# Kernel optimization log

Hardware: AMD Instinct MI355X
Metric: run time of the kernel (lower is better)

The kernel has to match this reference:

```python
import jax, jax.numpy as jnp
import numpy as np

P = 16           # patch size
D = 768          # embed / feature dim (= 3*P*P)
T = 8            # number of task vectors
H_META = 192     # MetaNet hidden (= D // 4)


def patchify(x):
    # x: [B, 3, H, W] -> [B, N, 3*P*P]
    B, C, H, W = x.shape
    x = x.reshape(B, C, H // P, P, W // P, P)
    x = x.transpose(0, 2, 4, 1, 3, 5)
    return x.reshape(B, (H // P) * (W // P), C * P * P)


def encode(W1, b1, W2, b2, x):
    # base functional encoder f(params, x): shared weights over the batch
    patches = patchify(x)                       # [B, N, D]
    h = jax.nn.relu(patches @ W1 + b1)          # [B, N, D]
    pooled = h.mean(axis=1)                     # [B, D]
    return pooled @ W2 + b2                     # [B, D]


def setup_inputs() -> dict:
    key = jax.random.key(0)
    ks = jax.random.split(key, 14)
    B = 64
    s = 0.02
    return {
        "x":   jax.random.normal(ks[0], (B, 3, 224, 224), jnp.float32),
        # base model params
        "W1":  jax.random.normal(ks[1], (D, D), jnp.float32) * s,
        "b1":  jax.random.normal(ks[2], (D,), jnp.float32) * s,
        "W2":  jax.random.normal(ks[3], (D, D), jnp.float32) * s,
        "b2":  jax.random.normal(ks[4], (D,), jnp.float32) * s,
        # task-vector deltas (stacked over T tasks)
        "dW1": jax.random.normal(ks[5], (T, D, D), jnp.float32) * s,
        "db1": jax.random.normal(ks[6], (T, D), jnp.float32) * s,
        "dW2": jax.random.normal(ks[7], (T, D, D), jnp.float32) * s,
        "db2": jax.random.normal(ks[8], (T, D), jnp.float32) * s,
        # MetaNet (Linear-ReLU-Linear); zero-init in the original, random here
        "mw1": jax.random.normal(ks[9], (D, H_META), jnp.float32) * s,
        "mb1": jax.random.normal(ks[10], (H_META,), jnp.float32) * s,
        "mw2": jax.random.normal(ks[11], (H_META, T), jnp.float32) * s,
        "mb2": jax.random.normal(ks[12], (T,), jnp.float32) * s,
    }


def reference(x, W1, b1, W2, b2, dW1, db1, dW2, db2, mw1, mb1, mw2, mb2):
    # 1) base features with frozen base model (torch.no_grad)
    base = jax.lax.stop_gradient(encode(W1, b1, W2, b2, x))       # [B, D]
    # 2) per-sample mixing coefficients via MetaNet
    coefs = jax.nn.relu(base @ mw1 + mb1) @ mw2 + mb2             # [B, T]
    # 3) per-sample mixed parameters: p + sum_t c[b,t] * dp[t]
    nW1 = W1 + jnp.einsum("bt,tij->bij", coefs, dW1)              # [B, D, D]
    nb1 = b1 + coefs @ db1                                        # [B, D]
    nW2 = W2 + jnp.einsum("bt,tij->bij", coefs, dW2)              # [B, D, D]
    nb2 = b2 + coefs @ db2                                        # [B, D]
    # 4) batched per-sample forward with the mixed weights
    patches = patchify(x)                                         # [B, N, D]
    h = jax.nn.relu(jnp.einsum("bnd,bde->bne", patches, nW1) + nb1[:, None, :])
    pooled = h.mean(axis=1)                                       # [B, D]
    out = jnp.einsum("bd,bde->be", pooled, nW2) + nb2             # [B, D]
    return out
```

## Files before the change

kernel.cpp:

```cpp
#include <hip/hip_runtime.h>
#include <hip/hip_bf16.h>


typedef __bf16 bf16x8 __attribute__((ext_vector_type(8)));
typedef float f32x4 __attribute__((ext_vector_type(4)));

struct alignas(16) BF8 { __hip_bfloat16 h[8]; };

constexpr int BATCH = 64;
constexpr int NP    = 196;
constexpr int NPAD  = 256;
constexpr int DIM   = 768;
constexpr int NT    = 8;
constexpr int HM    = 192;
constexpr size_t MSZ = (size_t)DIM * DIM;

__global__ void k_patchify(const float* __restrict__ x, __hip_bfloat16* __restrict__ A) {
  int idx  = blockIdx.x * blockDim.x + threadIdx.x;
  int col4 = idx % (DIM / 4);
  int row  = idx / (DIM / 4);
  int d = col4 * 4;
  int b = row >> 8;
  int n = row & 255;
  __hip_bfloat16 tmp[4];
  if (n < NP) {
    int hp = n / 14, wp = n % 14;
    int c  = d >> 8;
    int rr = d & 255;
    int i = rr >> 4, j = rr & 15;
    const float* src = x + ((((size_t)b * 3 + c) * 224 + hp * 16 + i) * 224 + wp * 16 + j);
    float4 f = *(const float4*)src;
    tmp[0] = __float2bfloat16(f.x);
    tmp[1] = __float2bfloat16(f.y);
    tmp[2] = __float2bfloat16(f.z);
    tmp[3] = __float2bfloat16(f.w);
  } else {
    tmp[0] = tmp[1] = tmp[2] = tmp[3] = __float2bfloat16(0.0f);
  }
  *(ushort4*)(A + (size_t)row * DIM + d) = *(ushort4*)tmp;
}

__global__ void k_transpose_cast(const float* __restrict__ W1, const float* __restrict__ dW1,
                                 const float* __restrict__ W2, const float* __restrict__ dW2,
                                 __hip_bfloat16* __restrict__ WT) {
  __shared__ float tile[32][33];
  int mat = blockIdx.z;
  const float* src;
  if      (mat == 0) src = W1;
  else if (mat <= 8) src = dW1 + (size_t)(mat - 1) * MSZ;
  else if (mat == 9) src = W2;
  else               src = dW2 + (size_t)(mat - 10) * MSZ;
  int n0 = blockIdx.x * 32;
  int k0 = blockIdx.y * 32;
  int tx = threadIdx.x & 31, ty = threadIdx.x >> 5;
#pragma unroll
  for (int r = ty; r < 32; r += 8)
    tile[r][tx] = src[(size_t)(k0 + r) * DIM + n0 + tx];
  __syncthreads();
  __hip_bfloat16* dst = WT + (size_t)mat * MSZ;
#pragma unroll
  for (int r = ty; r < 32; r += 8)
    dst[(size_t)(n0 + r) * DIM + k0 + tx] = __float2bfloat16(tile[tx][r]);
}

constexpr int LDP = 40;

__global__ __launch_bounds__(256, 2)
void k_gemm_pool(const __hip_bfloat16* __restrict__ A,
                 const __hip_bfloat16* __restrict__ WT,
                 const float* __restrict__ b1,
                 const float* __restrict__ db1,
                 const float* __restrict__ coefs,
                 __hip_bfloat16* __restrict__ pooled) {
  __shared__ __hip_bfloat16 Asl[256][LDP];
  __shared__ __hip_bfloat16 Bsl[64][LDP];
  __shared__ float biasl[64];
  __shared__ float cl[NT];
  __shared__ float red[4][64];

  int b  = blockIdx.x;
  int n0 = blockIdx.y * 64;
  int tid = threadIdx.x;

  if (tid < NT) cl[tid] = coefs ? coefs[b * NT + tid] : 0.0f;
  __syncthreads();
  if (tid < 64) {
    float bias = b1[n0 + tid];
    if (coefs) {
#pragma unroll
      for (int t = 0; t < NT; t++) bias += cl[t] * db1[t * DIM + n0 + tid];
    }
    biasl[tid] = bias;
  }

  int wave = tid >> 6, lane = tid & 63;
  int quad = lane >> 4, l16 = lane & 15;
  f32x4 acc[4][4] = {};
  const __hip_bfloat16* Ag = A + (size_t)b * (NPAD * DIM);

  for (int k0 = 0; k0 < DIM; k0 += 32) {
    {
      int kl = (tid & 3) * 8;
      int r  = tid >> 2;
#pragma unroll
      for (int p = 0; p < 4; p++, r += 64)
        *(uint4*)(&Asl[r][kl]) = *(const uint4*)(Ag + (size_t)r * DIM + k0 + kl);
    }
    {
      int kl = (tid & 3) * 8;
      int nl = tid >> 2;
      const __hip_bfloat16* p0 = WT + (size_t)(n0 + nl) * DIM + k0 + kl;
      if (coefs) {
        BF8 w = *(const BF8*)p0;
        float m[8];
#pragma unroll
        for (int i = 0; i < 8; i++) m[i] = __bfloat162float(w.h[i]);
#pragma unroll
        for (int t = 0; t < NT; t++) {
          BF8 dv = *(const BF8*)(p0 + (size_t)(1 + t) * MSZ);
          float c = cl[t];
#pragma unroll
          for (int i = 0; i < 8; i++) m[i] += c * __bfloat162float(dv.h[i]);
        }
        BF8 o;
#pragma unroll
        for (int i = 0; i < 8; i++) o.h[i] = __float2bfloat16(m[i]);
        *(BF8*)(&Bsl[nl][kl]) = o;
      } else {
        *(uint4*)(&Bsl[nl][kl]) = *(const uint4*)p0;
      }
    }
    __syncthreads();
    int m0 = wave * 64;
    bf16x8 af[4], bfr[4];
#pragma unroll
    for (int mf = 0; mf < 4; mf++)
      af[mf] = *(const bf16x8*)(&Asl[m0 + mf * 16 + l16][quad * 8]);
#pragma unroll
    for (int nf = 0; nf < 4; nf++)
      bfr[nf] = *(const bf16x8*)(&Bsl[nf * 16 + l16][quad * 8]);
#pragma unroll
    for (int mf = 0; mf < 4; mf++)
#pragma unroll
      for (int nf = 0; nf < 4; nf++)
        acc[mf][nf] = __builtin_amdgcn_mfma_f32_16x16x32_bf16(af[mf], bfr[nf], acc[mf][nf], 0, 0, 0);
    __syncthreads();
  }

  int m0 = wave * 64;
  float colsum[4];
#pragma unroll
  for (int nf = 0; nf < 4; nf++) {
    float bias = biasl[nf * 16 + l16];
    float s = 0.0f;
#pragma unroll
    for (int mf = 0; mf < 4; mf++) {
      int rowbase = m0 + mf * 16 + quad * 4;
#pragma unroll
      for (int r = 0; r < 4; r++) {
        if (rowbase + r < NP) s += fmaxf(acc[mf][nf][r] + bias, 0.0f);
      }
    }
    s += __shfl_xor(s, 16, 64);
    s += __shfl_xor(s, 32, 64);
    colsum[nf] = s;
  }
  if (lane < 16) {
#pragma unroll
    for (int nf = 0; nf < 4; nf++) red[wave][nf * 16 + lane] = colsum[nf];
  }
  __syncthreads();
  if (tid < 64) {
    float s = red[0][tid] + red[1][tid] + red[2][tid] + red[3][tid];
    pooled[(size_t)b * DIM + n0 + tid] = __float2bfloat16(s * (1.0f / 196.0f));
  }
}

__global__ __launch_bounds__(256, 2)
void k_gemm2(const __hip_bfloat16* __restrict__ Abf,
             const __hip_bfloat16* __restrict__ WT,
             int matbase,
             const float* __restrict__ bias,
             float* __restrict__ Y) {
  __shared__ __hip_bfloat16 Asl[64][LDP];
  __shared__ __hip_bfloat16 Bsl[64][LDP];
  int n0  = blockIdx.x * 64;
  int mat = blockIdx.y;
  int tid = threadIdx.x, wave = tid >> 6, lane = tid & 63;
  int quad = lane >> 4, l16 = lane & 15;
  f32x4 acc[4] = {};
  const __hip_bfloat16* Wm = WT + (size_t)(matbase + mat) * MSZ;
  for (int k0 = 0; k0 < DIM; k0 += 32) {
    int kl = (tid & 3) * 8;
    int r  = tid >> 2;
    *(uint4*)(&Asl[r][kl]) = *(const uint4*)(Abf + (size_t)r * DIM + k0 + kl);
    *(uint4*)(&Bsl[r][kl]) = *(const uint4*)(Wm + (size_t)(n0 + r) * DIM + k0 + kl);
    __syncthreads();
    bf16x8 bfr = *(const bf16x8*)(&Bsl[wave * 16 + l16][quad * 8]);
#pragma unroll
    for (int mf = 0; mf < 4; mf++) {
      bf16x8 af = *(const bf16x8*)(&Asl[mf * 16 + l16][quad * 8]);
      acc[mf] = __builtin_amdgcn_mfma_f32_16x16x32_bf16(af, bfr, acc[mf], 0, 0, 0);
    }
    __syncthreads();
  }
#pragma unroll
  for (int mf = 0; mf < 4; mf++) {
#pragma unroll
    for (int r = 0; r < 4; r++) {
      int row = mf * 16 + quad * 4 + r;
      int col = n0 + wave * 16 + l16;
      float v = acc[mf][r];
      if (bias) v += bias[col];
      Y[((size_t)mat * 64 + row) * DIM + col] = v;
    }
  }
}

__global__ void k_metanet(const float* __restrict__ base,
                          const float* __restrict__ mw1, const float* __restrict__ mb1,
                          const float* __restrict__ mw2, const float* __restrict__ mb2,
                          float* __restrict__ coefs) {
  __shared__ float bl[DIM];
  __shared__ float hl[HM];
  int b = blockIdx.x, tid = threadIdx.x;
  for (int i = tid; i < DIM; i += HM) bl[i] = base[(size_t)b * DIM + i];
  __syncthreads();
  float s = mb1[tid];
  for (int k = 0; k < DIM; k++) s += bl[k] * mw1[(size_t)k * HM + tid];
  hl[tid] = fmaxf(s, 0.0f);
  __syncthreads();
  if (tid < NT) {
    float c = mb2[tid];
    for (int j = 0; j < HM; j++) c += hl[j] * mw2[(size_t)j * NT + tid];
    coefs[b * NT + tid] = c;
  }
}

__global__ void k_combine(const float* __restrict__ Y,
                          const float* __restrict__ coefs,
                          const float* __restrict__ b2,
                          const float* __restrict__ db2,
                          float* __restrict__ out) {
  int idx = blockIdx.x * 256 + threadIdx.x;
  int b = idx / DIM, e = idx % DIM;
  float v = Y[(size_t)b * DIM + e] + b2[e];
#pragma unroll
  for (int t = 0; t < NT; t++) {
    float c = coefs[b * NT + t];
    v += c * (Y[((size_t)(1 + t) * 64 + b) * DIM + e] + db2[(size_t)t * DIM + e]);
  }
  out[idx] = v;
}

extern "C" void kernel_launch(void* const* d_in, const int* in_sizes, int n_in,
                              void* d_out, int out_size, void* d_ws, size_t ws_size,
                              hipStream_t stream) {
  const float* x   = (const float*)d_in[0];
  const float* W1  = (const float*)d_in[1];
  const float* b1  = (const float*)d_in[2];
  const float* W2  = (const float*)d_in[3];
  const float* b2  = (const float*)d_in[4];
  const float* dW1 = (const float*)d_in[5];
  const float* db1 = (const float*)d_in[6];
  const float* dW2 = (const float*)d_in[7];
  const float* db2 = (const float*)d_in[8];
  const float* mw1 = (const float*)d_in[9];
  const float* mb1 = (const float*)d_in[10];
  const float* mw2 = (const float*)d_in[11];
  const float* mb2 = (const float*)d_in[12];
  float* out = (float*)d_out;

  char* ws = (char*)d_ws;
  __hip_bfloat16* A_bf     = (__hip_bfloat16*)(ws);
  __hip_bfloat16* WT       = (__hip_bfloat16*)(ws + 25165824);
  __hip_bfloat16* pooledA  = (__hip_bfloat16*)(ws + 46399488);
  float*          base     = (float*)         (ws + 46497792);
  float*          coefs    = (float*)         (ws + 46694400);
  __hip_bfloat16* pooledB  = (__hip_bfloat16*)(ws + 46696448);
  float*          Y        = (float*)         (ws + 46794752);
  (void)ws_size; (void)in_sizes; (void)n_in; (void)out_size;

  k_patchify<<<dim3((BATCH * NPAD * (DIM / 4)) / 256), 256, 0, stream>>>(x, A_bf);
  k_transpose_cast<<<dim3(24, 24, 18), 256, 0, stream>>>(W1, dW1, W2, dW2, WT);
  k_gemm_pool<<<dim3(BATCH, DIM / 64), 256, 0, stream>>>(A_bf, WT, b1, db1, nullptr, pooledA);
  k_gemm2<<<dim3(DIM / 64, 1), 256, 0, stream>>>(pooledA, WT, 9, b2, base);
  k_metanet<<<dim3(BATCH), HM, 0, stream>>>(base, mw1, mb1, mw2, mb2, coefs);
  k_gemm_pool<<<dim3(BATCH, DIM / 64), 256, 0, stream>>>(A_bf, WT, b1, db1, coefs, pooledB);
  k_gemm2<<<dim3(DIM / 64, 9), 256, 0, stream>>>(pooledB, WT, 9, nullptr, Y);
  k_combine<<<dim3((BATCH * DIM) / 256), 256, 0, stream>>>(Y, coefs, b2, db2, out);
}
```

Baseline: 315.2 us.

## Precompute per-sample mixed W1, retile pooled GEMM, fuse base GEMM with MetaNet

When the workspace is large enough, a new k_mix kernel materialises the per-sample mixed W1 in bf16 once. The second pooled GEMM can then read it directly instead of recombining 9 matrices inside every tile. The pooled GEMM moves to 128-column tiles with a 64-wide K step, an XOR-swizzled LDS layout, a split over row blocks, and fp32 atomic pooling, which needs a memset first. The base W2 projection and the MetaNet are fused into one fp32 kernel. k_gemm2 now converts fp32 pooled input inline. The precompute writes about 75MB of mixed weights, which adds memory traffic, and the fp32 projection kernel may be slow.

```diff
diff --git a/kernel.cpp b/kernel.cpp
--- a/kernel.cpp
+++ b/kernel.cpp
@@ -4,25 +4,25 @@
 
 typedef __bf16 bf16x8 __attribute__((ext_vector_type(8)));
 typedef float f32x4 __attribute__((ext_vector_type(4)));
-
-struct alignas(16) BF8 { __hip_bfloat16 h[8]; };
+typedef __hip_bfloat16 bf16;
+
+struct alignas(16) BF8 { bf16 h[8]; };
 
 constexpr int BATCH = 64;
 constexpr int NP    = 196;
 constexpr int NPAD  = 256;
 constexpr int DIM   = 768;
 constexpr int NT    = 8;
-constexpr int HM    = 192;
 constexpr size_t MSZ = (size_t)DIM * DIM;
 
-__global__ void k_patchify(const float* __restrict__ x, __hip_bfloat16* __restrict__ A) {
+__global__ void k_patchify(const float* __restrict__ x, bf16* __restrict__ A) {
   int idx  = blockIdx.x * blockDim.x + threadIdx.x;
   int col4 = idx % (DIM / 4);
   int row  = idx / (DIM / 4);
   int d = col4 * 4;
   int b = row >> 8;
   int n = row & 255;
-  __hip_bfloat16 tmp[4];
+  bf16 tmp[4];
   if (n < NP) {
     int hp = n / 14, wp = n % 14;
     int c  = d >> 8;
@@ -42,7 +42,7 @@
 
 __global__ void k_transpose_cast(const float* __restrict__ W1, const float* __restrict__ dW1,
                                  const float* __restrict__ W2, const float* __restrict__ dW2,
-                                 __hip_bfloat16* __restrict__ WT) {
+                                 bf16* __restrict__ WT) {
   __shared__ float tile[32][33];
   int mat = blockIdx.z;
   const float* src;
@@ -57,34 +57,95 @@
   for (int r = ty; r < 32; r += 8)
     tile[r][tx] = src[(size_t)(k0 + r) * DIM + n0 + tx];
   __syncthreads();
-  __hip_bfloat16* dst = WT + (size_t)mat * MSZ;
+  bf16* dst = WT + (size_t)mat * MSZ;
 #pragma unroll
   for (int r = ty; r < 32; r += 8)
     dst[(size_t)(n0 + r) * DIM + k0 + tx] = __float2bfloat16(tile[tx][r]);
 }
 
-constexpr int LDP = 40;
-
-__global__ __launch_bounds__(256, 2)
-void k_gemm_pool(const __hip_bfloat16* __restrict__ A,
-                 const __hip_bfloat16* __restrict__ WT,
+__global__ void k_mix(const bf16* __restrict__ WT, const float* __restrict__ coefs,
+                      bf16* __restrict__ nW1T) {
+  __shared__ float cls[BATCH * NT];
+  int tid = threadIdx.x;
+  cls[tid]       = coefs[tid];
+  cls[tid + 256] = coefs[tid + 256];
+  __syncthreads();
+  size_t g  = (size_t)blockIdx.x * 128 + (tid & 127);
+  int    b0 = (tid >> 7) * 32;
+  const bf16* p = WT + g * 8;
+  BF8 wv = *(const BF8*)p;
+  float w[8], d[NT][8];
+#pragma unroll
+  for (int i = 0; i < 8; i++) w[i] = __bfloat162float(wv.h[i]);
+#pragma unroll
+  for (int t = 0; t < NT; t++) {
+    BF8 dv = *(const BF8*)(p + (size_t)(1 + t) * MSZ);
+#pragma unroll
+    for (int i = 0; i < 8; i++) d[t][i] = __bfloat162float(dv.h[i]);
+  }
+  for (int b = b0; b < b0 + 32; b++) {
+    float m[8];
+#pragma unroll
+    for (int i = 0; i < 8; i++) m[i] = w[i];
+#pragma unroll
+    for (int t = 0; t < NT; t++) {
+      float c = cls[b * NT + t];
+#pragma unroll
+      for (int i = 0; i < 8; i++) m[i] += c * d[t][i];
+    }
+    BF8 o;
+#pragma unroll
+    for (int i = 0; i < 8; i++) o.h[i] = __float2bfloat16(m[i]);
+    *(BF8*)(nW1T + (size_t)b * MSZ + g * 8) = o;
+  }
+}
+
+
+template<int MFR>
+__device__ __forceinline__ void gp_kloop(const bf16* As, const bf16* Bs, int wrow0, int wc,
+                                         int quad, int l16, f32x4 acc[4][4]) {
+#pragma unroll
+  for (int ks = 0; ks < 2; ks++) {
+    bf16x8 bfr[4];
+#pragma unroll
+    for (int nf = 0; nf < 4; nf++) {
+      int rrow = wc * 64 + nf * 16 + l16;
+      bfr[nf] = *(const bf16x8*)(Bs + (size_t)(rrow * 8 + ((ks * 4 + quad) ^ (rrow & 7))) * 8);
+    }
+#pragma unroll
+    for (int mf = 0; mf < MFR; mf++) {
+      int arow = wrow0 + mf * 16 + l16;
+      bf16x8 af = *(const bf16x8*)(As + (size_t)(arow * 8 + ((ks * 4 + quad) ^ (arow & 7))) * 8);
+#pragma unroll
+      for (int nf = 0; nf < 4; nf++)
+        acc[mf][nf] = __builtin_amdgcn_mfma_f32_16x16x32_bf16(af, bfr[nf], acc[mf][nf], 0, 0, 0);
+    }
+  }
+}
+
+__global__ __launch_bounds__(256, 3)
+void k_gemm_pool(const bf16* __restrict__ A,
+                 const bf16* __restrict__ Bsrc,
+                 int perSample,
                  const float* __restrict__ b1,
                  const float* __restrict__ db1,
                  const float* __restrict__ coefs,
-                 __hip_bfloat16* __restrict__ pooled) {
-  __shared__ __hip_bfloat16 Asl[256][LDP];
-  __shared__ __hip_bfloat16 Bsl[64][LDP];
-  __shared__ float biasl[64];
+                 int inlineMix,
+                 float* __restrict__ pooled) {
+  __shared__ uint4 AslU[128 * 8];
+  __shared__ uint4 BslU[128 * 8];
+  __shared__ float biasl[128];
   __shared__ float cl[NT];
-  __shared__ float red[4][64];
+  __shared__ float red[2][128];
 
   int b  = blockIdx.x;
-  int n0 = blockIdx.y * 64;
+  int rb = blockIdx.y;
+  int n0 = blockIdx.z * 128;
   int tid = threadIdx.x;
 
   if (tid < NT) cl[tid] = coefs ? coefs[b * NT + tid] : 0.0f;
   __syncthreads();
-  if (tid < 64) {
+  if (tid < 128) {
     float bias = b1[n0 + tid];
     if (coefs) {
 #pragma unroll
@@ -93,24 +154,35 @@
     biasl[tid] = bias;
   }
 
+  int rows    = rb ? 96 : 128;
+  int rowbase = rb * 128;
+  const bf16* Ag = A + ((size_t)b * NPAD + rowbase) * DIM;
+  const bf16* Bg = Bsrc + (perSample ? (size_t)b * MSZ : 0);
+
   int wave = tid >> 6, lane = tid & 63;
   int quad = lane >> 4, l16 = lane & 15;
+  int wr = wave >> 1, wc = wave & 1;
+  int wrow0 = wr * (rb ? 48 : 64);
+
   f32x4 acc[4][4] = {};
-  const __hip_bfloat16* Ag = A + (size_t)b * (NPAD * DIM);
-
-  for (int k0 = 0; k0 < DIM; k0 += 32) {
-    {
-      int kl = (tid & 3) * 8;
-      int r  = tid >> 2;
-#pragma unroll
-      for (int p = 0; p < 4; p++, r += 64)
-        *(uint4*)(&Asl[r][kl]) = *(const uint4*)(Ag + (size_t)r * DIM + k0 + kl);
-    }
-    {
-      int kl = (tid & 3) * 8;
-      int nl = tid >> 2;
-      const __hip_bfloat16* p0 = WT + (size_t)(n0 + nl) * DIM + k0 + kl;
-      if (coefs) {
+  int nA = rows * 8;
+
+  for (int k0 = 0; k0 < DIM; k0 += 64) {
+    for (int g = tid; g < nA; g += 256) {
+      int r = g >> 3, c = g & 7;
+      uint4 v = *(const uint4*)(Ag + (size_t)r * DIM + k0 + c * 8);
+      AslU[r * 8 + (c ^ (r & 7))] = v;
+    }
+    if (!inlineMix) {
+      for (int g = tid; g < 1024; g += 256) {
+        int r = g >> 3, c = g & 7;
+        uint4 v = *(const uint4*)(Bg + (size_t)(n0 + r) * DIM + k0 + c * 8);
+        BslU[r * 8 + (c ^ (r & 7))] = v;
+      }
+    } else {
+      for (int g = tid; g < 1024; g += 256) {
+        int r = g >> 3, c = g & 7;
+        const bf16* p0 = Bg + (size_t)(n0 + r) * DIM + k0 + c * 8;
         BF8 w = *(const BF8*)p0;
         float m[8];
 #pragma unroll
@@ -118,47 +190,35 @@
 #pragma unroll
         for (int t = 0; t < NT; t++) {
           BF8 dv = *(const BF8*)(p0 + (size_t)(1 + t) * MSZ);
-          float c = cl[t];
-#pragma unroll
-          for (int i = 0; i < 8; i++) m[i] += c * __bfloat162float(dv.h[i]);
+          float c2 = cl[t];
+#pragma unroll
+          for (int i = 0; i < 8; i++) m[i] += c2 * __bfloat162float(dv.h[i]);
         }
         BF8 o;
 #pragma unroll
         for (int i = 0; i < 8; i++) o.h[i] = __float2bfloat16(m[i]);
-        *(BF8*)(&Bsl[nl][kl]) = o;
-      } else {
-        *(uint4*)(&Bsl[nl][kl]) = *(const uint4*)p0;
+        BslU[r * 8 + (c ^ (r & 7))] = *(uint4*)&o;
       }
     }
     __syncthreads();
-    int m0 = wave * 64;
-    bf16x8 af[4], bfr[4];
-#pragma unroll
-    for (int mf = 0; mf < 4; mf++)
-      af[mf] = *(const bf16x8*)(&Asl[m0 + mf * 16 + l16][quad * 8]);
-#pragma unroll
-    for (int nf = 0; nf < 4; nf++)
-      bfr[nf] = *(const bf16x8*)(&Bsl[nf * 16 + l16][quad * 8]);
-#pragma unroll
-    for (int mf = 0; mf < 4; mf++)
-#pragma unroll
-      for (int nf = 0; nf < 4; nf++)
-        acc[mf][nf] = __builtin_amdgcn_mfma_f32_16x16x32_bf16(af[mf], bfr[nf], acc[mf][nf], 0, 0, 0);
+    const bf16* As = (const bf16*)AslU;
+    const bf16* Bs = (const bf16*)BslU;
+    if (rb == 0) gp_kloop<4>(As, Bs, wrow0, wc, quad, l16, acc);
+    else         gp_kloop<3>(As, Bs, wrow0, wc, quad, l16, acc);
     __syncthreads();
   }
 
-  int m0 = wave * 64;
+  int mfr = rb ? 3 : 4;
   float colsum[4];
 #pragma unroll
   for (int nf = 0; nf < 4; nf++) {
-    float bias = biasl[nf * 16 + l16];
+    float bias = biasl[wc * 64 + nf * 16 + l16];
     float s = 0.0f;
-#pragma unroll
-    for (int mf = 0; mf < 4; mf++) {
-      int rowbase = m0 + mf * 16 + quad * 4;
+    for (int mf = 0; mf < mfr; mf++) {
+      int rbase = rowbase + wrow0 + mf * 16 + quad * 4;
 #pragma unroll
       for (int r = 0; r < 4; r++) {
-        if (rowbase + r < NP) s += fmaxf(acc[mf][nf][r] + bias, 0.0f);
+        if (rbase + r < NP) s += fmaxf(acc[mf][nf][r] + bias, 0.0f);
       }
     }
     s += __shfl_xor(s, 16, 64);
@@ -167,40 +227,91 @@
   }
   if (lane < 16) {
 #pragma unroll
-    for (int nf = 0; nf < 4; nf++) red[wave][nf * 16 + lane] = colsum[nf];
-  }
-  __syncthreads();
-  if (tid < 64) {
-    float s = red[0][tid] + red[1][tid] + red[2][tid] + red[3][tid];
-    pooled[(size_t)b * DIM + n0 + tid] = __float2bfloat16(s * (1.0f / 196.0f));
+    for (int nf = 0; nf < 4; nf++) red[wr][wc * 64 + nf * 16 + lane] = colsum[nf];
+  }
+  __syncthreads();
+  if (tid < 128) {
+    float s = red[0][tid] + red[1][tid];
+    atomicAdd(pooled + (size_t)b * DIM + n0 + tid, s * (1.0f / 196.0f));
+  }
+}
+
+__global__ void k_base_metanet(const float* __restrict__ pooled,
+                               const float* __restrict__ W2,
+                               const float* __restrict__ b2,
+                               const float* __restrict__ mw1, const float* __restrict__ mb1,
+                               const float* __restrict__ mw2, const float* __restrict__ mb2,
+                               float* __restrict__ coefs) {
+  __shared__ float pl[DIM];
+  __shared__ float basel[DIM];
+  __shared__ float hl[192];
+  int b = blockIdx.x, tid = threadIdx.x;
+  for (int i = tid; i < DIM; i += 256) pl[i] = pooled[(size_t)b * DIM + i];
+  __syncthreads();
+  float s0 = b2[tid], s1 = b2[tid + 256], s2 = b2[tid + 512];
+  for (int k = 0; k < DIM; k++) {
+    float pv = pl[k];
+    const float* wr = W2 + (size_t)k * DIM;
+    s0 += pv * wr[tid];
+    s1 += pv * wr[tid + 256];
+    s2 += pv * wr[tid + 512];
+  }
+  basel[tid] = s0; basel[tid + 256] = s1; basel[tid + 512] = s2;
+  __syncthreads();
+  if (tid < 192) {
+    float h = mb1[tid];
+    for (int k = 0; k < DIM; k++) h += basel[k] * mw1[(size_t)k * 192 + tid];
+    hl[tid] = fmaxf(h, 0.0f);
+  }
+  __syncthreads();
+  if (tid < NT) {
+    float c = mb2[tid];
+    for (int j = 0; j < 192; j++) c += hl[j] * mw2[(size_t)j * NT + tid];
+    coefs[b * NT + tid] = c;
   }
 }
 
 __global__ __launch_bounds__(256, 2)
-void k_gemm2(const __hip_bfloat16* __restrict__ Abf,
-             const __hip_bfloat16* __restrict__ WT,
-             int matbase,
-             const float* __restrict__ bias,
+void k_gemm2(const float* __restrict__ Af,
+             const bf16* __restrict__ WT,
              float* __restrict__ Y) {
-  __shared__ __hip_bfloat16 Asl[64][LDP];
-  __shared__ __hip_bfloat16 Bsl[64][LDP];
+  __shared__ uint4 AslU[64 * 8];
+  __shared__ uint4 BslU[64 * 8];
   int n0  = blockIdx.x * 64;
   int mat = blockIdx.y;
   int tid = threadIdx.x, wave = tid >> 6, lane = tid & 63;
   int quad = lane >> 4, l16 = lane & 15;
   f32x4 acc[4] = {};
-  const __hip_bfloat16* Wm = WT + (size_t)(matbase + mat) * MSZ;
-  for (int k0 = 0; k0 < DIM; k0 += 32) {
-    int kl = (tid & 3) * 8;
-    int r  = tid >> 2;
-    *(uint4*)(&Asl[r][kl]) = *(const uint4*)(Abf + (size_t)r * DIM + k0 + kl);
-    *(uint4*)(&Bsl[r][kl]) = *(const uint4*)(Wm + (size_t)(n0 + r) * DIM + k0 + kl);
+  const bf16* Wm = WT + (size_t)(9 + mat) * MSZ;
+  for (int k0 = 0; k0 < DIM; k0 += 64) {
+#pragma unroll
+    for (int i = 0; i < 2; i++) {
+      int g = tid + i * 256;
+      int r = g >> 3, c = g & 7;
+      const float* src = Af + (size_t)r * DIM + k0 + c * 8;
+      float4 xa = ((const float4*)src)[0];
+      float4 xb = ((const float4*)src)[1];
+      BF8 o;
+      o.h[0] = __float2bfloat16(xa.x); o.h[1] = __float2bfloat16(xa.y);
+      o.h[2] = __float2bfloat16(xa.z); o.h[3] = __float2bfloat16(xa.w);
+      o.h[4] = __float2bfloat16(xb.x); o.h[5] = __float2bfloat16(xb.y);
+      o.h[6] = __float2bfloat16(xb.z); o.h[7] = __float2bfloat16(xb.w);
+      AslU[r * 8 + (c ^ (r & 7))] = *(uint4*)&o;
+      BslU[r * 8 + (c ^ (r & 7))] = *(const uint4*)(Wm + (size_t)(n0 + r) * DIM + k0 + c * 8);
+    }
     __syncthreads();
-    bf16x8 bfr = *(const bf16x8*)(&Bsl[wave * 16 + l16][quad * 8]);
-#pragma unroll
-    for (int mf = 0; mf < 4; mf++) {
-      bf16x8 af = *(const bf16x8*)(&Asl[mf * 16 + l16][quad * 8]);
-      acc[mf] = __builtin_amdgcn_mfma_f32_16x16x32_bf16(af, bfr, acc[mf], 0, 0, 0);
+    const bf16* As = (const bf16*)AslU;
+    const bf16* Bs = (const bf16*)BslU;
+#pragma unroll
+    for (int ks = 0; ks < 2; ks++) {
+      int brow = wave * 16 + l16;
+      bf16x8 bfr = *(const bf16x8*)(Bs + (size_t)(brow * 8 + ((ks * 4 + quad) ^ (brow & 7))) * 8);
+#pragma unroll
+      for (int mf = 0; mf < 4; mf++) {
+        int arow = mf * 16 + l16;
+        bf16x8 af = *(const bf16x8*)(As + (size_t)(arow * 8 + ((ks * 4 + quad) ^ (arow & 7))) * 8);
+        acc[mf] = __builtin_amdgcn_mfma_f32_16x16x32_bf16(af, bfr, acc[mf], 0, 0, 0);
+      }
     }
     __syncthreads();
   }
@@ -210,30 +321,8 @@
     for (int r = 0; r < 4; r++) {
       int row = mf * 16 + quad * 4 + r;
       int col = n0 + wave * 16 + l16;
-      float v = acc[mf][r];
-      if (bias) v += bias[col];
-      Y[((size_t)mat * 64 + row) * DIM + col] = v;
-    }
-  }
-}
-
-__global__ void k_metanet(const float* __restrict__ base,
-                          const float* __restrict__ mw1, const float* __restrict__ mb1,
-                          const float* __restrict__ mw2, const float* __restrict__ mb2,
-                          float* __restrict__ coefs) {
-  __shared__ float bl[DIM];
-  __shared__ float hl[HM];
-  int b = blockIdx.x, tid = threadIdx.x;
-  for (int i = tid; i < DIM; i += HM) bl[i] = base[(size_t)b * DIM + i];
-  __syncthreads();
-  float s = mb1[tid];
-  for (int k = 0; k < DIM; k++) s += bl[k] * mw1[(size_t)k * HM + tid];
-  hl[tid] = fmaxf(s, 0.0f);
-  __syncthreads();
-  if (tid < NT) {
-    float c = mb2[tid];
-    for (int j = 0; j < HM; j++) c += hl[j] * mw2[(size_t)j * NT + tid];
-    coefs[b * NT + tid] = c;
+      Y[((size_t)mat * 64 + row) * DIM + col] = acc[mf][r];
+    }
   }
 }
 
@@ -270,23 +359,31 @@
   const float* mw2 = (const float*)d_in[11];
   const float* mb2 = (const float*)d_in[12];
   float* out = (float*)d_out;
+  (void)in_sizes; (void)n_in; (void)out_size;
 
   char* ws = (char*)d_ws;
-  __hip_bfloat16* A_bf     = (__hip_bfloat16*)(ws);
-  __hip_bfloat16* WT       = (__hip_bfloat16*)(ws + 25165824);
-  __hip_bfloat16* pooledA  = (__hip_bfloat16*)(ws + 46399488);
-  float*          base     = (float*)         (ws + 46497792);
-  float*          coefs    = (float*)         (ws + 46694400);
-  __hip_bfloat16* pooledB  = (__hip_bfloat16*)(ws + 46696448);
-  float*          Y        = (float*)         (ws + 46794752);
-  (void)ws_size; (void)in_sizes; (void)n_in; (void)out_size;
+  bf16*  A_bf    = (bf16*) (ws);
+  bf16*  WT      = (bf16*) (ws + 25165824);
+  float* pooledA = (float*)(ws + 46399488);
+  float* pooledB = (float*)(ws + 46596096);
+  float* coefs   = (float*)(ws + 46792704);
+  float* Y       = (float*)(ws + 46794752);
+  bf16*  nW1T    = (bf16*) (ws + 48564224);
+  const size_t NEED_BIG = 124061696;
+  bool big = ws_size >= NEED_BIG;
+
+  hipMemsetAsync(pooledA, 0, 2 * 196608, stream);
 
   k_patchify<<<dim3((BATCH * NPAD * (DIM / 4)) / 256), 256, 0, stream>>>(x, A_bf);
   k_transpose_cast<<<dim3(24, 24, 18), 256, 0, stream>>>(W1, dW1, W2, dW2, WT);
-  k_gemm_pool<<<dim3(BATCH, DIM / 64), 256, 0, stream>>>(A_bf, WT, b1, db1, nullptr, pooledA);
-  k_gemm2<<<dim3(DIM / 64, 1), 256, 0, stream>>>(pooledA, WT, 9, b2, base);
-  k_metanet<<<dim3(BATCH), HM, 0, stream>>>(base, mw1, mb1, mw2, mb2, coefs);
-  k_gemm_pool<<<dim3(BATCH, DIM / 64), 256, 0, stream>>>(A_bf, WT, b1, db1, coefs, pooledB);
-  k_gemm2<<<dim3(DIM / 64, 9), 256, 0, stream>>>(pooledB, WT, 9, nullptr, Y);
+  k_gemm_pool<<<dim3(BATCH, 2, 6), 256, 0, stream>>>(A_bf, WT, 0, b1, db1, nullptr, 0, pooledA);
+  k_base_metanet<<<dim3(BATCH), 256, 0, stream>>>(pooledA, W2, b2, mw1, mb1, mw2, mb2, coefs);
+  if (big) {
+    k_mix<<<dim3(576), 256, 0, stream>>>(WT, coefs, nW1T);
+    k_gemm_pool<<<dim3(BATCH, 2, 6), 256, 0, stream>>>(A_bf, nW1T, 1, b1, db1, coefs, 0, pooledB);
+  } else {
+    k_gemm_pool<<<dim3(BATCH, 2, 6), 256, 0, stream>>>(A_bf, WT, 0, b1, db1, coefs, 1, pooledB);
+  }
+  k_gemm2<<<dim3(DIM / 64, 9), 256, 0, stream>>>(pooledB, WT, Y);
   k_combine<<<dim3((BATCH * DIM) / 256), 256, 0, stream>>>(Y, coefs, b2, db2, out);
 }
```

New measurement: 788.5 us. 150% more time.
